# Kernel optimization log

Hardware: AMD Instinct MI355X
Metric: run time of the kernel (lower is better)

Reference implementation:

```python
import jax, jax.numpy as jnp
import numpy as np

N, A, M = 2, 360, 512
NP, PS = 32, 64


def _rampfilter(size):
    n = np.concatenate((np.arange(1, size / 2 + 1, 2, dtype=int),
                        np.arange(size / 2 - 1, 0, -2, dtype=int)))
    f = np.zeros(size)
    f[0] = 0.25
    f[1::2] = -1 / (np.pi * n) ** 2
    return 2 * np.real(np.fft.fft(f))


def setup_inputs() -> dict:
    rng = np.random.default_rng(0)
    sino = rng.standard_normal((N, 1, A, M))
    # ramp filtering (done in __init__ of the torch module, filtered=True)
    final_width = max(64, int(2 ** np.ceil(np.log2(2 * M))))
    pad = final_width - M
    filt = _rampfilter(final_width)
    sino_p = np.pad(sino, ((0, 0), (0, 0), (0, 0), (0, pad)))
    sino_f = np.real(np.fft.ifft(np.fft.fft(sino_p, axis=-1) * filt, axis=-1))[..., :M]
    # patch centers sampled uniformly inside the reconstruction circle
    cx, cy = [], []
    while sum(len(a) for a in cx) < NP:
        x_ = rng.random(NP) * M
        y_ = rng.random(NP) * M
        m = (x_ - M / 2) ** 2 + (y_ - M / 2) ** 2 <= (M / 2) ** 2
        cx.append(x_[m]); cy.append(y_[m])
    centers_x = np.concatenate(cx)[:NP]
    centers_y = np.concatenate(cy)[:NP]
    theta = np.linspace(0.0, np.pi, A, endpoint=False)
    return {
        'sinogram': jnp.asarray(sino_f, jnp.float32),
        'theta': jnp.asarray(theta, jnp.float32),
        'centers_x': jnp.asarray(centers_x, jnp.float32),
        'centers_y': jnp.asarray(centers_y, jnp.float32),
    }


def reference(sinogram, theta, centers_x, centers_y):
    n, _, a, m = sinogram.shape
    sino = sinogram[:, 0]                                  # (N, A, M)
    half = (m - 1) / 2.0
    x = jnp.arange(PS, dtype=sinogram.dtype) - PS / 2.0
    # patch grids (torch meshgrid 'ij'): gX varies along rows, gy along cols
    gX = (x[:, None] + jnp.zeros((PS,), sinogram.dtype)[None, :])[None] + centers_x[:, None, None]
    gy = (jnp.zeros((PS,), sinogram.dtype)[:, None] + x[None, :])[None] + centers_y[:, None, None]
    gX = gX / half - 1.0                                   # (NP, PS, PS), normalized
    gy = gy / half - 1.0
    ct, st = jnp.cos(theta), jnp.sin(theta)                # (A,)
    # rotated detector coordinate per angle: (NP, A, PS, PS)
    xg = gX[:, None] * ct[None, :, None, None] - gy[:, None] * st[None, :, None, None]
    # grid_sample bilinear along M with align_corners=True, zero padding
    u = (xg + 1.0) * half
    i0 = jnp.floor(u)
    w = u - i0
    i0i = i0.astype(jnp.int32)
    i1i = i0i + 1
    w0 = jnp.where((i0i >= 0) & (i0i <= m - 1), 1.0 - w, 0.0)
    w1 = jnp.where((i1i >= 0) & (i1i <= m - 1), w, 0.0)
    i0c = jnp.clip(i0i, 0, m - 1)
    i1c = jnp.clip(i1i, 0, m - 1)
    a_idx = jnp.arange(a)[None, :, None, None]
    g0 = sino[:, a_idx, i0c]                               # (N, NP, A, PS, PS)
    g1 = sino[:, a_idx, i1c]
    recon = (g0 * w0[None] + g1 * w1[None]).sum(axis=2)    # sum over angles -> (N, NP, PS, PS)
    mask = ((gX ** 2 + gy ** 2) <= 1.0).astype(recon.dtype)
    recon = recon * mask[None]
    return recon * (np.pi / (2.0 * a))
```

## Files before the change

kernel.cpp:

```cpp
#include <hip/hip_runtime.h>
#include <math.h>

#define N_  2
#define A_  360
#define M_  512
#define NP_ 32
#define PS_ 64
#define HALF_A 180
#define W_  24

__global__ __launch_bounds__(512) void fbp_kernel(
    const float* __restrict__ sino,
    const float* __restrict__ theta,
    const float* __restrict__ cxs,
    const float* __restrict__ cys,
    float* __restrict__ out)
{
    __shared__ float2 win2[A_ * W_];
    __shared__ alignas(16) float csA[A_];
    __shared__ alignas(16) float syA[A_];
    __shared__ alignas(16) float ofA[A_];
    __shared__ float red[256];

    const float half = 255.5f;
    const int tid = threadIdx.x;

    const int bid    = blockIdx.x;
    const int region = bid & 15;
    const int p      = (bid >> 4) & (NP_ - 1);
    const int n      = bid >> 9;
    const int ri     = (region >> 2) << 4;
    const int rj     = (region &  3) << 4;

    const float cx = cxs[p];
    const float cy = cys[p];

    const float gX0 = ((float)(ri      - PS_ / 2) + cx) / half - 1.0f;
    const float gX1 = ((float)(ri + 15 - PS_ / 2) + cx) / half - 1.0f;
    const float gy0 = ((float)(rj      - PS_ / 2) + cy) / half - 1.0f;
    const float gy1 = ((float)(rj + 15 - PS_ / 2) + cy) / half - 1.0f;

    if (tid < A_) {
        const float th  = theta[tid];
        const float csx = cosf(th) * half;
        const float csy = sinf(th) * half;
        const float t0  = fmaf(-gy0, csy, half);
        const float t1  = fmaf(-gy1, csy, half);
        const float u00 = fmaf(gX0, csx, t0);
        const float u10 = fmaf(gX1, csx, t0);
        const float u01 = fmaf(gX0, csx, t1);
        const float u11 = fmaf(gX1, csx, t1);
        const float lof = floorf(fminf(fminf(u00, u10), fminf(u01, u11)));
        csA[tid] = csx;
        syA[tid] = csy;
        ofA[tid] = half - lof;
    }
    __syncthreads();

    const float* __restrict__ srow = sino + n * (A_ * M_);
    for (int e = tid; e < A_ * W_; e += 512) {
        const int a  = e / W_;
        const int k  = e - a * W_;
        const int lo = (int)(half - ofA[a]);
        const int i0 = min(max(lo + k,     0), M_ - 1);
        const int i1 = min(max(lo + k + 1, 0), M_ - 1);
        const float g0 = srow[a * M_ + i0];
        const float g1 = srow[a * M_ + i1];
        win2[e] = make_float2(g0, g1 - g0);
    }
    __syncthreads();

    const int team = tid >> 8;
    const int t    = tid & 255;
    const int i    = ri + (t >> 4);
    const int j    = rj + (t & 15);

    const float gX  = ((float)(i - PS_ / 2) + cx) / half - 1.0f;
    const float gy  = ((float)(j - PS_ / 2) + cy) / half - 1.0f;
    const float ngy = -gy;

    const int gbase = team * (HALF_A / 4);
    const float4* __restrict__ cs4 = (const float4*)csA;
    const float4* __restrict__ sy4 = (const float4*)syA;
    const float4* __restrict__ of4 = (const float4*)ofA;

    float accG = 0.0f;
    float accW = 0.0f;
    const float2* wp0 = win2 + team * (HALF_A * W_);

    #pragma unroll 3
    for (int g = 0; g < HALF_A / 4; ++g) {
        const float4 c4 = cs4[gbase + g];
        const float4 s4 = sy4[gbase + g];
        const float4 o4 = of4[gbase + g];
        const float2* wp = wp0 + g * (4 * W_);

        {
            float u = fmaf(gX, c4.x, fmaf(ngy, s4.x, o4.x));
            u = fminf(fmaxf(u, 0.0f), 22.999f);
            const float2 gg = wp[(int)u];
            accG += gg.x;  accW = fmaf(__builtin_amdgcn_fractf(u), gg.y, accW);
        }
        {
            float u = fmaf(gX, c4.y, fmaf(ngy, s4.y, o4.y));
            u = fminf(fmaxf(u, 0.0f), 22.999f);
            const float2 gg = wp[W_ + (int)u];
            accG += gg.x;  accW = fmaf(__builtin_amdgcn_fractf(u), gg.y, accW);
        }
        {
            float u = fmaf(gX, c4.z, fmaf(ngy, s4.z, o4.z));
            u = fminf(fmaxf(u, 0.0f), 22.999f);
            const float2 gg = wp[2 * W_ + (int)u];
            accG += gg.x;  accW = fmaf(__builtin_amdgcn_fractf(u), gg.y, accW);
        }
        {
            float u = fmaf(gX, c4.w, fmaf(ngy, s4.w, o4.w));
            u = fminf(fmaxf(u, 0.0f), 22.999f);
            const float2 gg = wp[3 * W_ + (int)u];
            accG += gg.x;  accW = fmaf(__builtin_amdgcn_fractf(u), gg.y, accW);
        }
    }

    const float part = accG + accW;
    if (team == 1) red[t] = part;
    __syncthreads();
    if (team == 0) {
        const float inside = (fmaf(gX, gX, gy * gy) <= 1.0f) ? 1.0f : 0.0f;
        const float scale  = (float)(M_PI / (2.0 * (double)A_));
        out[(((n * NP_) + p) * PS_ + i) * PS_ + j] =
            (part + red[t]) * inside * scale;
    }
}

extern "C" void kernel_launch(void* const* d_in, const int* in_sizes, int n_in,
                              void* d_out, int out_size, void* d_ws, size_t ws_size,
                              hipStream_t stream) {
    const float* sino  = (const float*)d_in[0];
    const float* theta = (const float*)d_in[1];
    const float* cxs   = (const float*)d_in[2];
    const float* cys   = (const float*)d_in[3];
    float* out = (float*)d_out;

    const int blocks = N_ * NP_ * (PS_ * PS_ / 256);
    fbp_kernel<<<dim3(blocks), dim3(512), 0, stream>>>(sino, theta, cxs, cys, out);
}
```

Measured before the change: 31.19 us.

## Shrink pixel tiles to 8x8 with eight angle teams per block

Each block now covers an 8x8 pixel region instead of 16x16. Its 512 threads are split into eight wavefront-sized teams, and each team handles 45 of the 360 angles. The smaller footprint halves the per-angle sinogram window from 24 to 12 entries, which shrinks shared-memory staging per block and quadruples the block count for better occupancy. In exchange, blocks load the window four times as often in total, and an eight-way reduction through shared memory (reusing the window buffer) replaces the earlier two-way one.

```diff
diff --git a/kernel.cpp b/kernel.cpp
--- a/kernel.cpp
+++ b/kernel.cpp
@@ -6,8 +6,11 @@
 #define M_  512
 #define NP_ 32
 #define PS_ 64
-#define HALF_A 180
-#define W_  24
+#define RT_ 8
+#define W_  12
+#define TEAMS 8
+#define TA_ 45
+#define TPAD 48
 
 __global__ __launch_bounds__(512) void fbp_kernel(
     const float* __restrict__ sino,
@@ -17,28 +20,26 @@
     float* __restrict__ out)
 {
     __shared__ float2 win2[A_ * W_];
-    __shared__ alignas(16) float csA[A_];
-    __shared__ alignas(16) float syA[A_];
-    __shared__ alignas(16) float ofA[A_];
-    __shared__ float red[256];
+    __shared__ alignas(16) float2 csyT[TEAMS][TPAD];
+    __shared__ alignas(16) float  ofT[TEAMS][TPAD];
 
     const float half = 255.5f;
     const int tid = threadIdx.x;
 
     const int bid    = blockIdx.x;
-    const int region = bid & 15;
-    const int p      = (bid >> 4) & (NP_ - 1);
-    const int n      = bid >> 9;
-    const int ri     = (region >> 2) << 4;
-    const int rj     = (region &  3) << 4;
+    const int region = bid & 63;
+    const int p      = (bid >> 6) & (NP_ - 1);
+    const int n      = bid >> 11;
+    const int ri     = (region >> 3) << 3;
+    const int rj     = (region &  7) << 3;
 
     const float cx = cxs[p];
     const float cy = cys[p];
 
-    const float gX0 = ((float)(ri      - PS_ / 2) + cx) / half - 1.0f;
-    const float gX1 = ((float)(ri + 15 - PS_ / 2) + cx) / half - 1.0f;
-    const float gy0 = ((float)(rj      - PS_ / 2) + cy) / half - 1.0f;
-    const float gy1 = ((float)(rj + 15 - PS_ / 2) + cy) / half - 1.0f;
+    const float gX0 = ((float)(ri     - PS_ / 2) + cx) / half - 1.0f;
+    const float gX1 = ((float)(ri + 7 - PS_ / 2) + cx) / half - 1.0f;
+    const float gy0 = ((float)(rj     - PS_ / 2) + cy) / half - 1.0f;
+    const float gy1 = ((float)(rj + 7 - PS_ / 2) + cy) / half - 1.0f;
 
     if (tid < A_) {
         const float th  = theta[tid];
@@ -51,9 +52,10 @@
         const float u01 = fmaf(gX0, csx, t1);
         const float u11 = fmaf(gX1, csx, t1);
         const float lof = floorf(fminf(fminf(u00, u10), fminf(u01, u11)));
-        csA[tid] = csx;
-        syA[tid] = csy;
-        ofA[tid] = half - lof;
+        const int   tm  = tid / TA_;
+        const int   al  = tid - tm * TA_;
+        csyT[tm][al] = make_float2(csx, csy);
+        ofT[tm][al]  = half - lof;
     }
     __syncthreads();
 
@@ -61,7 +63,9 @@
     for (int e = tid; e < A_ * W_; e += 512) {
         const int a  = e / W_;
         const int k  = e - a * W_;
-        const int lo = (int)(half - ofA[a]);
+        const int tm = a / TA_;
+        const int al = a - tm * TA_;
+        const int lo = (int)(half - ofT[tm][al]);
         const int i0 = min(max(lo + k,     0), M_ - 1);
         const int i1 = min(max(lo + k + 1, 0), M_ - 1);
         const float g0 = srow[a * M_ + i0];
@@ -70,65 +74,75 @@
     }
     __syncthreads();
 
-    const int team = tid >> 8;
-    const int t    = tid & 255;
-    const int i    = ri + (t >> 4);
-    const int j    = rj + (t & 15);
+    const int team = tid >> 6;
+    const int lane = tid & 63;
+    const int i    = ri + (lane >> 3);
+    const int j    = rj + (lane & 7);
 
     const float gX  = ((float)(i - PS_ / 2) + cx) / half - 1.0f;
     const float gy  = ((float)(j - PS_ / 2) + cy) / half - 1.0f;
     const float ngy = -gy;
 
-    const int gbase = team * (HALF_A / 4);
-    const float4* __restrict__ cs4 = (const float4*)csA;
-    const float4* __restrict__ sy4 = (const float4*)syA;
-    const float4* __restrict__ of4 = (const float4*)ofA;
+    const float4* __restrict__ csy4 = (const float4*)&csyT[team][0];
+    const float4* __restrict__ of4  = (const float4*)&ofT[team][0];
+    const float2* __restrict__ wbase = win2 + team * (TA_ * W_);
 
     float accG = 0.0f;
     float accW = 0.0f;
-    const float2* wp0 = win2 + team * (HALF_A * W_);
 
-    #pragma unroll 3
-    for (int g = 0; g < HALF_A / 4; ++g) {
-        const float4 c4 = cs4[gbase + g];
-        const float4 s4 = sy4[gbase + g];
-        const float4 o4 = of4[gbase + g];
-        const float2* wp = wp0 + g * (4 * W_);
+    #pragma unroll 4
+    for (int g = 0; g < 11; ++g) {
+        const float4 cA = csy4[2 * g];
+        const float4 cB = csy4[2 * g + 1];
+        const float4 o4 = of4[g];
+        const float2* wp = wbase + g * (4 * W_);
 
         {
-            float u = fmaf(gX, c4.x, fmaf(ngy, s4.x, o4.x));
-            u = fminf(fmaxf(u, 0.0f), 22.999f);
+            float u = fmaf(gX, cA.x, fmaf(ngy, cA.y, o4.x));
+            u = fminf(fmaxf(u, 0.0f), 11.999f);
             const float2 gg = wp[(int)u];
             accG += gg.x;  accW = fmaf(__builtin_amdgcn_fractf(u), gg.y, accW);
         }
         {
-            float u = fmaf(gX, c4.y, fmaf(ngy, s4.y, o4.y));
-            u = fminf(fmaxf(u, 0.0f), 22.999f);
+            float u = fmaf(gX, cA.z, fmaf(ngy, cA.w, o4.y));
+            u = fminf(fmaxf(u, 0.0f), 11.999f);
             const float2 gg = wp[W_ + (int)u];
             accG += gg.x;  accW = fmaf(__builtin_amdgcn_fractf(u), gg.y, accW);
         }
         {
-            float u = fmaf(gX, c4.z, fmaf(ngy, s4.z, o4.z));
-            u = fminf(fmaxf(u, 0.0f), 22.999f);
+            float u = fmaf(gX, cB.x, fmaf(ngy, cB.y, o4.z));
+            u = fminf(fmaxf(u, 0.0f), 11.999f);
             const float2 gg = wp[2 * W_ + (int)u];
             accG += gg.x;  accW = fmaf(__builtin_amdgcn_fractf(u), gg.y, accW);
         }
         {
-            float u = fmaf(gX, c4.w, fmaf(ngy, s4.w, o4.w));
-            u = fminf(fmaxf(u, 0.0f), 22.999f);
+            float u = fmaf(gX, cB.z, fmaf(ngy, cB.w, o4.w));
+            u = fminf(fmaxf(u, 0.0f), 11.999f);
             const float2 gg = wp[3 * W_ + (int)u];
             accG += gg.x;  accW = fmaf(__builtin_amdgcn_fractf(u), gg.y, accW);
         }
     }
+    {
+        const float2 cst = csyT[team][44];
+        const float  of  = ofT[team][44];
+        float u = fmaf(gX, cst.x, fmaf(ngy, cst.y, of));
+        u = fminf(fmaxf(u, 0.0f), 11.999f);
+        const float2 gg = wbase[44 * W_ + (int)u];
+        accG += gg.x;  accW = fmaf(__builtin_amdgcn_fractf(u), gg.y, accW);
+    }
 
-    const float part = accG + accW;
-    if (team == 1) red[t] = part;
+    float part = accG + accW;
+
+    __syncthreads();
+    float* red = (float*)win2;
+    if (team != 0) red[(team - 1) * 64 + lane] = part;
     __syncthreads();
     if (team == 0) {
+        #pragma unroll
+        for (int q = 0; q < 7; ++q) part += red[q * 64 + lane];
         const float inside = (fmaf(gX, gX, gy * gy) <= 1.0f) ? 1.0f : 0.0f;
         const float scale  = (float)(M_PI / (2.0 * (double)A_));
-        out[(((n * NP_) + p) * PS_ + i) * PS_ + j] =
-            (part + red[t]) * inside * scale;
+        out[(((n * NP_) + p) * PS_ + i) * PS_ + j] = part * inside * scale;
     }
 }
 
@@ -141,6 +155,6 @@
     const float* cys   = (const float*)d_in[3];
     float* out = (float*)d_out;
 
-    const int blocks = N_ * NP_ * (PS_ * PS_ / 256);
+    const int blocks = N_ * NP_ * ((PS_ / RT_) * (PS_ / RT_));
     fbp_kernel<<<dim3(blocks), dim3(512), 0, stream>>>(sino, theta, cxs, cys, out);
 }
```

Measured after the change: 38.18 us. +22.4%, slower.
